# Performance work log

Hardware: AMD Instinct MI355X
Metric: run time of the kernel (lower is better)

## Reference

```python
import jax, jax.numpy as jnp
import numpy as np

K_GRID = 20          # grid side -> n1 = 400 nodes, n2 = 760 edges
CONTEXT = 512
HIDDEN = 2 * CONTEXT # per module: hidden_dim = 2*context_size
BATCH = 4096
RHO = 1.0            # ADMM penalty
N_ITERS = 50         # fixed ADMM iterations (differentiable unroll)


def _grid_incidence(k):
    """Node-arc incidence of a k x k grid DAG (right + down edges)."""
    n = k * k
    edges = []
    for i in range(k):
        for j in range(k):
            u = i * k + j
            if j + 1 < k:
                edges.append((u, i * k + j + 1))
            if i + 1 < k:
                edges.append((u, (i + 1) * k + j))
    m = len(edges)
    A = np.zeros((n, m), np.float32)
    for e, (u, v) in enumerate(edges):
        A[u, e] = 1.0   # outflow
        A[v, e] = -1.0  # inflow
    b = np.zeros(n, np.float32)
    b[0] = 1.0      # source
    b[n - 1] = -1.0 # sink
    return A, b


def setup_inputs() -> dict:
    key = jax.random.key(0)
    k_d, k_w1, k_b1, k_w2, k_b2 = jax.random.split(key, 5)
    A_np, b_np = _grid_incidence(K_GRID)
    n2 = A_np.shape[1]
    d = jax.random.normal(k_d, (BATCH, CONTEXT), dtype=jnp.float32)
    s1 = 1.0 / np.sqrt(CONTEXT)
    s2 = 1.0 / np.sqrt(HIDDEN)
    W1 = jax.random.uniform(k_w1, (HIDDEN, CONTEXT), jnp.float32, -s1, s1)
    b1 = jax.random.uniform(k_b1, (HIDDEN,), jnp.float32, -s1, s1)
    W2 = jax.random.uniform(k_w2, (n2, HIDDEN), jnp.float32, -s2, s2)
    b2 = jax.random.uniform(k_b2, (n2,), jnp.float32, -s2, s2)
    return {"d": d, "W1": W1, "b1": b1, "W2": W2, "b2": b2,
            "A": jnp.asarray(A_np), "b_eq": jnp.asarray(b_np)}


def reference(d, W1, b1, W2, b2, A, b_eq):
    # MLP router: fc_1 -> LeakyReLU(0.1) -> fc_2
    h = d @ W1.T + b1
    h = jnp.where(h >= 0, h, 0.1 * h)
    w = h @ W2.T + b2  # [B, n2] edge costs

    # QP: min_x w^T x + 0.5||x||^2  s.t.  A x = b_eq, x >= 0
    # Batched ADMM with equality-constrained x-update (KKT solve via pinv(AA^T)).
    M = jnp.linalg.pinv(A @ A.T)  # [n1, n1], symmetric
    z = jnp.zeros_like(w)
    u = jnp.zeros_like(w)
    x = jnp.zeros_like(w)

    def step(carry, _):
        x, z, u = carry
        v = RHO * (z - u) - w                       # [B, n2]
        nu = (v @ A.T - (1.0 + RHO) * b_eq) @ M     # [B, n1] dual of Ax=b
        x = (v - nu @ A) / (1.0 + RHO)              # satisfies A x = b
        z = jnp.maximum(x + u, 0.0)                 # projection onto x >= 0
        u = u + x - z
        return (x, z, u), None

    (x, z, u), _ = jax.lax.scan(step, (x, z, u), None, length=N_ITERS)
    return x  # [B, n2], primal solution (matches CvxpyLayer's variable x)
```

## Files before the change

### kernel.cpp

```cpp
#include <hip/hip_runtime.h>

#define KG 20
#define N1 400
#define N2 760
#define BATCH 4096
#define NITER 50

typedef __attribute__((ext_vector_type(8))) short bf16x8;
typedef __attribute__((ext_vector_type(4))) float f32x4;

#define CBAR() asm volatile("" ::: "memory")

__device__ __forceinline__ float bf2f(unsigned short u) {
    unsigned int x = ((unsigned int)u) << 16;
    union { unsigned int i; float f; } c; c.i = x; return c.f;
}
__device__ __forceinline__ unsigned short f2bf(float f) {
    union { float f; unsigned int i; } c; c.f = f;
    unsigned int r = c.i + 0x7FFFu + ((c.i >> 16) & 1u);
    return (unsigned short)(r >> 16);
}
__device__ __forceinline__ unsigned pk_bf16(float lo, float hi) {
    unsigned r;
    asm("v_cvt_pk_bf16_f32 %0, %1, %2" : "=v"(r) : "v"(lo), "v"(hi));
    return r;
}

constexpr double CPI = 3.14159265358979323846;
constexpr double ccos(double x) {
    constexpr double TP = 6.28318530717958647692;
    long long k = (long long)(x / TP);
    double r = x - (double)k * TP;
    if (r > CPI)  r -= TP;
    if (r < -CPI) r += TP;
    double r2 = r * r, term = 1.0, s = 1.0;
    for (int n = 1; n <= 15; ++n) { term *= -r2 / ((2.0 * n - 1.0) * (2.0 * n)); s += term; }
    return s;
}
struct Tbl { float phi[10][20]; float lam[20]; };
constexpr Tbl mk_tbl() {
    Tbl t{};
    for (int i = 0; i < 10; ++i)
        for (int a = 0; a < 20; ++a) {
            double na = (a == 0) ? 0.22360679774997896964 : 0.31622776601683793320;
            t.phi[i][a] = (float)(na * ccos(CPI * (double)a * ((double)i + 0.5) / 20.0));
        }
    for (int a = 0; a < 20; ++a) t.lam[a] = (float)(2.0 - 2.0 * ccos(CPI * (double)a / 20.0));
    return t;
}
static constexpr Tbl TB = mk_tbl();

__device__ __forceinline__ int detect_flag(const float* beqf) {
    float v = beqf[0];
    return (v > 0.5f && v < 1.5f) ? 0 : 1;
}

__global__ __launch_bounds__(256) void cvt_inputs(
        const void* __restrict__ src0, const void* __restrict__ src1,
        unsigned short* __restrict__ dst0, unsigned short* __restrict__ dst1,
        const float* __restrict__ beqf) {
    const int f = detect_flag(beqf);
    const int nv0 = (4096 * 512) / 4, nv1 = (1024 * 512) / 4;
    int idx = blockIdx.x * 256 + threadIdx.x;
    if (idx >= nv0 + nv1) return;
    const void* s; unsigned short* dptr; int k;
    if (idx < nv0) { s = src0; dptr = dst0; k = idx; }
    else           { s = src1; dptr = dst1; k = idx - nv0; }
    if (f) {
        ((uint2*)dptr)[k] = ((const uint2*)s)[k];
    } else {
        float4 v = ((const float4*)s)[k];
        uint2 p; p.x = pk_bf16(v.x, v.y); p.y = pk_bf16(v.z, v.w);
        ((uint2*)dptr)[k] = p;
    }
}

template<bool LEAKY>
__global__ __launch_bounds__(256) void gemm_bt_bf16(
        const unsigned short* __restrict__ A,
        const void* __restrict__ B,
        const void* __restrict__ biasRaw,
        unsigned short* __restrict__ C,
        int M, int N, int K, const float* __restrict__ beqf, int bUseFlag) {
    __shared__ unsigned short As[64 * 34];
    __shared__ unsigned short Bs[64 * 34];
    const int f   = detect_flag(beqf);
    const int bBf = bUseFlag ? f : 1;
    const int tid  = threadIdx.x;
    const int m0   = blockIdx.x * 64;
    const int n0   = blockIdx.y * 64;
    const int wave = tid >> 6, lane = tid & 63;
    const int wm   = (wave & 1) * 32, wn = (wave >> 1) * 32;
    const int fr   = lane & 15;
    const int kc   = (lane >> 4) * 8;

    const int ra = tid >> 2, ca = (tid & 3) * 8;
    const int rbg = (n0 + ra < N) ? (n0 + ra) : (N - 1);

    uint4 av, bv;
    auto load_tiles = [&](int k0) {
        size_t aoff = (size_t)(m0 + ra) * K + k0 + ca;
        av = *(const uint4*)&A[aoff];
        size_t boff = (size_t)rbg * K + k0 + ca;
        if (bBf) bv = *(const uint4*)&((const unsigned short*)B)[boff];
        else {
            const float* Bf = (const float*)B;
            float4 f0 = *(const float4*)&Bf[boff];
            float4 f1 = *(const float4*)&Bf[boff + 4];
            bv.x = pk_bf16(f0.x, f0.y);
            bv.y = pk_bf16(f0.z, f0.w);
            bv.z = pk_bf16(f1.x, f1.y);
            bv.w = pk_bf16(f1.z, f1.w);
        }
    };

    f32x4 acc[2][2];
#pragma unroll
    for (int a = 0; a < 2; a++)
#pragma unroll
        for (int b = 0; b < 2; b++) acc[a][b] = (f32x4){0.f, 0.f, 0.f, 0.f};

    load_tiles(0);
    for (int k0 = 0; k0 < K; k0 += 32) {
        *(uint4*)&As[ra * 34 + ca] = av;
        *(uint4*)&Bs[ra * 34 + ca] = bv;
        __syncthreads();

        int kn = (k0 + 32 < K) ? (k0 + 32) : k0;
        load_tiles(kn);

        bf16x8 af[2], bfm[2];
#pragma unroll
        for (int a = 0; a < 2; a++) af[a]  = *(const bf16x8*)&As[(wm + a * 16 + fr) * 34 + kc];
#pragma unroll
        for (int b = 0; b < 2; b++) bfm[b] = *(const bf16x8*)&Bs[(wn + b * 16 + fr) * 34 + kc];
#pragma unroll
        for (int a = 0; a < 2; a++)
#pragma unroll
            for (int b = 0; b < 2; b++)
                acc[a][b] = __builtin_amdgcn_mfma_f32_16x16x32_bf16(af[a], bfm[b], acc[a][b], 0, 0, 0);
        __syncthreads();
    }
#pragma unroll
    for (int a = 0; a < 2; a++)
#pragma unroll
        for (int b = 0; b < 2; b++) {
            int col = n0 + wn + b * 16 + (lane & 15);
            if (col < N) {
                float bs = f ? bf2f(((const unsigned short*)biasRaw)[col])
                             : ((const float*)biasRaw)[col];
#pragma unroll
                for (int r = 0; r < 4; r++) {
                    int row = m0 + wm + a * 16 + (lane >> 4) * 4 + r;
                    float v = acc[a][b][r] + bs;
                    if (LEAKY) v = v >= 0.f ? v : 0.1f * v;
                    C[(size_t)row * N + col] = f2bf(v);
                }
            }
        }
}

#define SREG 448
__global__ __launch_bounds__(64, 1) void admm_kernel(
        const unsigned short* __restrict__ wglob,
        void* __restrict__ out, const float* __restrict__ beqf) {
    __shared__ float buf[3 * SREG];

    const int lane = threadIdx.x;
    const int q    = (lane >= 40) ? 2 : (lane >= 20 ? 1 : 0);
    const int i    = lane - 20 * q;
    const int sample = blockIdx.x * 3 + q;
    const int flag = detect_flag(beqf);

    if (lane < 60 && sample < BATCH) {
        float* B = &buf[q * SREG];
        const size_t gb = (size_t)sample * N2;

        float wh[20], wv[20];
        if (i < 19) {
#pragma unroll
            for (int j = 0; j < 19; ++j) {
                wh[j] = bf2f(wglob[gb + 39 * i + 2 * j]);
                wv[j] = bf2f(wglob[gb + 39 * i + 2 * j + 1]);
            }
            wh[19] = 0.f;
            wv[19] = bf2f(wglob[gb + 39 * i + 38]);
        } else {
#pragma unroll
            for (int j = 0; j < 19; ++j) { wh[j] = bf2f(wglob[gb + 741 + j]); wv[j] = 0.f; }
            wh[19] = 0.f; wv[19] = 0.f;
        }

        float g[20];
        {
            float lamB = TB.lam[i];
#pragma unroll
            for (int a = 0; a < 20; ++a) g[a] = 1.f / (TB.lam[a] + lamB);
            if (i == 0) g[0] = 0.f;
        }

        float sh[20], sv[20];
#pragma unroll
        for (int j = 0; j < 20; ++j) { sh[j] = 0.f; sv[j] = 0.f; }

        const int rup = (i > 0)  ? i - 1 : 0;
        const int rdn = (i < 19) ? i + 1 : i;

#pragma unroll 1
        for (int it = 0; it < NITER; ++it) {
            float vh[20], vv[20];
#pragma unroll
            for (int j = 0; j < 20; ++j) {
                vh[j] = fabsf(sh[j]) - wh[j];
                vv[j] = fabsf(sv[j]) - wv[j];
            }
#pragma unroll
            for (int j = 0; j < 20; j += 4)
                *(f32x4*)&B[20 * i + j] = (f32x4){vv[j], vv[j + 1], vv[j + 2], vv[j + 3]};
            CBAR();
            float vvUp[20];
#pragma unroll
            for (int j = 0; j < 20; j += 4) {
                f32x4 t = *(f32x4*)&B[20 * rup + j];
                vvUp[j] = t[0]; vvUp[j + 1] = t[1]; vvUp[j + 2] = t[2]; vvUp[j + 3] = t[3];
            }
            CBAR();
            float r[20];
#pragma unroll
            for (int j = 0; j < 20; ++j) {
                float acc = ((j < 19) ? vh[j] : 0.f) + vv[j];
                if (j > 0) acc -= vh[j - 1];
                acc -= (i > 0) ? vvUp[j] : 0.f;
                r[j] = acc;
            }
            r[0]  -= (i == 0)  ? 2.f : 0.f;
            r[19] += (i == 19) ? 2.f : 0.f;

            float e[10], o[10];
#pragma unroll
            for (int jj = 0; jj < 10; ++jj) { e[jj] = r[jj] + r[19 - jj]; o[jj] = r[jj] - r[19 - jj]; }
#pragma unroll
            for (int b = 0; b < 20; ++b) {
                float a;
                if ((b & 1) == 0) {
                    a = e[0] * TB.phi[0][b];
#pragma unroll
                    for (int jj = 1; jj < 10; ++jj) a += e[jj] * TB.phi[jj][b];
                } else {
                    a = o[0] * TB.phi[0][b];
#pragma unroll
                    for (int jj = 1; jj < 10; ++jj) a += o[jj] * TB.phi[jj][b];
                }
                B[22 * b + i] = a;
            }
            CBAR();
            float t2[20];
#pragma unroll
            for (int k = 0; k < 20; k += 2) {
                float2 p = *(const float2*)&B[22 * i + k];
                t2[k] = p.x; t2[k + 1] = p.y;
            }
            CBAR();
            float e2[10], o2[10];
#pragma unroll
            for (int kk = 0; kk < 10; ++kk) { e2[kk] = t2[kk] + t2[19 - kk]; o2[kk] = t2[kk] - t2[19 - kk]; }
            float v2[20];
#pragma unroll
            for (int a = 0; a < 20; ++a) {
                float acc;
                if ((a & 1) == 0) {
                    acc = e2[0] * TB.phi[0][a];
#pragma unroll
                    for (int kk = 1; kk < 10; ++kk) acc += e2[kk] * TB.phi[kk][a];
                } else {
                    acc = o2[0] * TB.phi[0][a];
#pragma unroll
                    for (int kk = 1; kk < 10; ++kk) acc += o2[kk] * TB.phi[kk][a];
                }
                v2[a] = acc * g[a];
            }
#pragma unroll
            for (int II = 0; II < 10; ++II) {
                float E = v2[0] * TB.phi[II][0];
#pragma unroll
                for (int m = 1; m < 10; ++m) E += v2[2 * m] * TB.phi[II][2 * m];
                float O = v2[1] * TB.phi[II][1];
#pragma unroll
                for (int m = 1; m < 10; ++m) O += v2[2 * m + 1] * TB.phi[II][2 * m + 1];
                B[22 * II + i]        = E + O;
                B[22 * (19 - II) + i] = E - O;
            }
            CBAR();
            float t3[20];
#pragma unroll
            for (int b = 0; b < 20; b += 2) {
                float2 p = *(const float2*)&B[22 * i + b];
                t3[b] = p.x; t3[b + 1] = p.y;
            }
            CBAR();
            float nu[20];
#pragma unroll
            for (int JJ = 0; JJ < 10; ++JJ) {
                float E = t3[0] * TB.phi[JJ][0];
#pragma unroll
                for (int m = 1; m < 10; ++m) E += t3[2 * m] * TB.phi[JJ][2 * m];
                float O = t3[1] * TB.phi[JJ][1];
#pragma unroll
                for (int m = 1; m < 10; ++m) O += t3[2 * m + 1] * TB.phi[JJ][2 * m + 1];
                nu[JJ]      = E + O;
                nu[19 - JJ] = E - O;
            }
#pragma unroll
            for (int j = 0; j < 20; j += 4)
                *(f32x4*)&B[20 * i + j] = (f32x4){nu[j], nu[j + 1], nu[j + 2], nu[j + 3]};
            CBAR();
            float nuDn[20];
#pragma unroll
            for (int j = 0; j < 20; j += 4) {
                f32x4 t = *(f32x4*)&B[20 * rdn + j];
                nuDn[j] = t[0]; nuDn[j + 1] = t[1]; nuDn[j + 2] = t[2]; nuDn[j + 3] = t[3];
            }
            CBAR();
#pragma unroll
            for (int j = 0; j < 20; ++j) {
                float xv = 0.5f * (vv[j] - nu[j] + nuDn[j]);
                sv[j] = xv + fminf(sv[j], 0.f);
                float xh = 0.f;
                if (j < 19) {
                    xh = 0.5f * (vh[j] - nu[j] + nu[j + 1]);
                    sh[j] = xh + fminf(sh[j], 0.f);
                }
                if (it == NITER - 1) {
                    if (i < 19) {
                        if (j < 19) {
                            if (flag) {
                                ((unsigned short*)out)[gb + 39 * i + 2 * j]     = f2bf(xh);
                                ((unsigned short*)out)[gb + 39 * i + 2 * j + 1] = f2bf(xv);
                            } else {
                                ((float*)out)[gb + 39 * i + 2 * j]     = xh;
                                ((float*)out)[gb + 39 * i + 2 * j + 1] = xv;
                            }
                        } else {
                            if (flag) ((unsigned short*)out)[gb + 39 * i + 38] = f2bf(xv);
                            else      ((float*)out)[gb + 39 * i + 38] = xv;
                        }
                    } else if (j < 19) {
                        if (flag) ((unsigned short*)out)[gb + 741 + j] = f2bf(xh);
                        else      ((float*)out)[gb + 741 + j] = xh;
                    }
                }
            }
        }
    }
}

extern "C" void kernel_launch(void* const* d_in, const int* in_sizes, int n_in,
                              void* d_out, int out_size, void* d_ws, size_t ws_size,
                              hipStream_t stream) {
    (void)in_sizes; (void)n_in; (void)out_size; (void)ws_size;
    const void*  d   = d_in[0];
    const void*  W1  = d_in[1];
    const void*  b1  = d_in[2];
    const void*  W2  = d_in[3];
    const void*  b2  = d_in[4];
    const float* beq = (const float*)d_in[6];

    char* ws = (char*)d_ws;
    unsigned short* h_bf  = (unsigned short*)(ws);
    unsigned short* w_bf  = (unsigned short*)(ws + 8388608);
    unsigned short* d_bf  = (unsigned short*)(ws + 8388608);
    unsigned short* w1_bf = (unsigned short*)(ws + 12582912);

    cvt_inputs<<<2560, 256, 0, stream>>>(d, W1, d_bf, w1_bf, beq);

    gemm_bt_bf16<true ><<<dim3(64, 16), 256, 0, stream>>>(d_bf, w1_bf, b1, h_bf, 4096, 1024, 512,  beq, 0);
    gemm_bt_bf16<false><<<dim3(64, 12), 256, 0, stream>>>(h_bf, W2,    b2, w_bf, 4096, 760,  1024, beq, 1);

    admm_kernel<<<(BATCH + 2) / 3, 64, 0, stream>>>(w_bf, d_out, beq);
}
```

Before: 324.5 us.

## Fuse input conversion and both MLP GEMMs into one cooperative persistent kernel

Merges the bf16 conversion kernel and the two MLP GEMM launches into a single cooperative kernel of 512 persistent blocks. The blocks loop over GEMM tiles and use grid-wide syncs between phases. W2 is now pre-converted to bf16 in the conversion phase instead of inside the GEMM load loop. This targets launch overhead and the idle gaps between kernels, at the cost of grid syncs and a fixed grid of 512 blocks that may limit occupancy and load balance. The ADMM kernel, which likely dominates runtime, is left as it was.

```diff
diff --git a/kernel.cpp b/kernel.cpp
--- a/kernel.cpp
+++ b/kernel.cpp
@@ -1,4 +1,7 @@
 #include <hip/hip_runtime.h>
+#include <hip/hip_cooperative_groups.h>
+
+namespace cg = cooperative_groups;
 
 #define KG 20
 #define N1 400
@@ -55,109 +58,116 @@
     return (v > 0.5f && v < 1.5f) ? 0 : 1;
 }
 
-__global__ __launch_bounds__(256) void cvt_inputs(
-        const void* __restrict__ src0, const void* __restrict__ src1,
-        unsigned short* __restrict__ dst0, unsigned short* __restrict__ dst1,
-        const float* __restrict__ beqf) {
-    const int f = detect_flag(beqf);
-    const int nv0 = (4096 * 512) / 4, nv1 = (1024 * 512) / 4;
-    int idx = blockIdx.x * 256 + threadIdx.x;
-    if (idx >= nv0 + nv1) return;
-    const void* s; unsigned short* dptr; int k;
-    if (idx < nv0) { s = src0; dptr = dst0; k = idx; }
-    else           { s = src1; dptr = dst1; k = idx - nv0; }
-    if (f) {
-        ((uint2*)dptr)[k] = ((const uint2*)s)[k];
-    } else {
-        float4 v = ((const float4*)s)[k];
-        uint2 p; p.x = pk_bf16(v.x, v.y); p.y = pk_bf16(v.z, v.w);
-        ((uint2*)dptr)[k] = p;
-    }
-}
 
 template<bool LEAKY>
-__global__ __launch_bounds__(256) void gemm_bt_bf16(
+__device__ __forceinline__ void gemm_tiles(
         const unsigned short* __restrict__ A,
-        const void* __restrict__ B,
+        const unsigned short* __restrict__ Bm,
         const void* __restrict__ biasRaw,
         unsigned short* __restrict__ C,
-        int M, int N, int K, const float* __restrict__ beqf, int bUseFlag) {
-    __shared__ unsigned short As[64 * 34];
-    __shared__ unsigned short Bs[64 * 34];
-    const int f   = detect_flag(beqf);
-    const int bBf = bUseFlag ? f : 1;
-    const int tid  = threadIdx.x;
-    const int m0   = blockIdx.x * 64;
-    const int n0   = blockIdx.y * 64;
+        int M, int N, int K, int f,
+        unsigned short* As, unsigned short* Bs, int bId, int tid) {
+    const int tn   = (N + 63) >> 6;
+    const int ttot = (M >> 6) * tn;
     const int wave = tid >> 6, lane = tid & 63;
     const int wm   = (wave & 1) * 32, wn = (wave >> 1) * 32;
     const int fr   = lane & 15;
     const int kc   = (lane >> 4) * 8;
-
-    const int ra = tid >> 2, ca = (tid & 3) * 8;
-    const int rbg = (n0 + ra < N) ? (n0 + ra) : (N - 1);
-
-    uint4 av, bv;
-    auto load_tiles = [&](int k0) {
-        size_t aoff = (size_t)(m0 + ra) * K + k0 + ca;
-        av = *(const uint4*)&A[aoff];
-        size_t boff = (size_t)rbg * K + k0 + ca;
-        if (bBf) bv = *(const uint4*)&((const unsigned short*)B)[boff];
-        else {
-            const float* Bf = (const float*)B;
-            float4 f0 = *(const float4*)&Bf[boff];
-            float4 f1 = *(const float4*)&Bf[boff + 4];
-            bv.x = pk_bf16(f0.x, f0.y);
-            bv.y = pk_bf16(f0.z, f0.w);
-            bv.z = pk_bf16(f1.x, f1.y);
-            bv.w = pk_bf16(f1.z, f1.w);
-        }
-    };
-
-    f32x4 acc[2][2];
-#pragma unroll
-    for (int a = 0; a < 2; a++)
-#pragma unroll
-        for (int b = 0; b < 2; b++) acc[a][b] = (f32x4){0.f, 0.f, 0.f, 0.f};
-
-    load_tiles(0);
-    for (int k0 = 0; k0 < K; k0 += 32) {
-        *(uint4*)&As[ra * 34 + ca] = av;
-        *(uint4*)&Bs[ra * 34 + ca] = bv;
+    const int ra   = tid >> 2, ca = (tid & 3) * 8;
+
+    for (int t = bId; t < ttot; t += 512) {
+        const int m0  = (t / tn) * 64;
+        const int n0  = (t % tn) * 64;
+        const int rbg = (n0 + ra < N) ? (n0 + ra) : (N - 1);
+        const size_t abase = (size_t)(m0 + ra) * K + ca;
+        const size_t bbase = (size_t)rbg * K + ca;
+
+        uint4 av = *(const uint4*)&A[abase];
+        uint4 bv = *(const uint4*)&Bm[bbase];
+
+        f32x4 acc[2][2];
+#pragma unroll
+        for (int a = 0; a < 2; a++)
+#pragma unroll
+            for (int b = 0; b < 2; b++) acc[a][b] = (f32x4){0.f, 0.f, 0.f, 0.f};
+
+        for (int k0 = 0; k0 < K; k0 += 32) {
+            __syncthreads();
+            *(uint4*)&As[ra * 34 + ca] = av;
+            *(uint4*)&Bs[ra * 34 + ca] = bv;
+            __syncthreads();
+
+            int kn = (k0 + 32 < K) ? (k0 + 32) : k0;
+            av = *(const uint4*)&A[abase + kn];
+            bv = *(const uint4*)&Bm[bbase + kn];
+
+            bf16x8 af[2], bfm[2];
+#pragma unroll
+            for (int a = 0; a < 2; a++) af[a]  = *(const bf16x8*)&As[(wm + a * 16 + fr) * 34 + kc];
+#pragma unroll
+            for (int b = 0; b < 2; b++) bfm[b] = *(const bf16x8*)&Bs[(wn + b * 16 + fr) * 34 + kc];
+#pragma unroll
+            for (int a = 0; a < 2; a++)
+#pragma unroll
+                for (int b = 0; b < 2; b++)
+                    acc[a][b] = __builtin_amdgcn_mfma_f32_16x16x32_bf16(af[a], bfm[b], acc[a][b], 0, 0, 0);
+        }
         __syncthreads();
-
-        int kn = (k0 + 32 < K) ? (k0 + 32) : k0;
-        load_tiles(kn);
-
-        bf16x8 af[2], bfm[2];
-#pragma unroll
-        for (int a = 0; a < 2; a++) af[a]  = *(const bf16x8*)&As[(wm + a * 16 + fr) * 34 + kc];
-#pragma unroll
-        for (int b = 0; b < 2; b++) bfm[b] = *(const bf16x8*)&Bs[(wn + b * 16 + fr) * 34 + kc];
 #pragma unroll
         for (int a = 0; a < 2; a++)
 #pragma unroll
-            for (int b = 0; b < 2; b++)
-                acc[a][b] = __builtin_amdgcn_mfma_f32_16x16x32_bf16(af[a], bfm[b], acc[a][b], 0, 0, 0);
-        __syncthreads();
+            for (int b = 0; b < 2; b++) {
+                int col = n0 + wn + b * 16 + (lane & 15);
+                if (col < N) {
+                    float bs = f ? bf2f(((const unsigned short*)biasRaw)[col])
+                                 : ((const float*)biasRaw)[col];
+#pragma unroll
+                    for (int r = 0; r < 4; r++) {
+                        int row = m0 + wm + a * 16 + (lane >> 4) * 4 + r;
+                        float v = acc[a][b][r] + bs;
+                        if (LEAKY) v = v >= 0.f ? v : 0.1f * v;
+                        C[(size_t)row * N + col] = f2bf(v);
+                    }
+                }
+            }
     }
-#pragma unroll
-    for (int a = 0; a < 2; a++)
-#pragma unroll
-        for (int b = 0; b < 2; b++) {
-            int col = n0 + wn + b * 16 + (lane & 15);
-            if (col < N) {
-                float bs = f ? bf2f(((const unsigned short*)biasRaw)[col])
-                             : ((const float*)biasRaw)[col];
-#pragma unroll
-                for (int r = 0; r < 4; r++) {
-                    int row = m0 + wm + a * 16 + (lane >> 4) * 4 + r;
-                    float v = acc[a][b][r] + bs;
-                    if (LEAKY) v = v >= 0.f ? v : 0.1f * v;
-                    C[(size_t)row * N + col] = f2bf(v);
-                }
-            }
-        }
+}
+
+__global__ __launch_bounds__(256, 2) void mlp_fused(
+        const void* dRaw, const void* w1Raw, const void* w2Raw,
+        const void* b1Raw, const void* b2Raw,
+        unsigned short* d_bf, unsigned short* w1_bf, unsigned short* w2_bf,
+        unsigned short* h_bf, unsigned short* w_bf,
+        const float* beqf) {
+    __shared__ unsigned short As[64 * 34];
+    __shared__ unsigned short Bs[64 * 34];
+    const int f   = detect_flag(beqf);
+    const int tid = threadIdx.x;
+    const int b   = blockIdx.x;
+
+    {
+        const int nv0 = (4096 * 512) / 4;
+        const int nv1 = (1024 * 512) / 4;
+        const int nv2 = (760 * 1024) / 4;
+        const int total = nv0 + nv1 + nv2;
+        for (int idx = b * 256 + tid; idx < total; idx += 512 * 256) {
+            const void* s; unsigned short* dst; int k;
+            if (idx < nv0)             { s = dRaw;  dst = d_bf;  k = idx; }
+            else if (idx < nv0 + nv1)  { s = w1Raw; dst = w1_bf; k = idx - nv0; }
+            else                       { s = w2Raw; dst = w2_bf; k = idx - nv0 - nv1; }
+            if (f) {
+                ((uint2*)dst)[k] = ((const uint2*)s)[k];
+            } else {
+                float4 v = ((const float4*)s)[k];
+                uint2 p; p.x = pk_bf16(v.x, v.y); p.y = pk_bf16(v.z, v.w);
+                ((uint2*)dst)[k] = p;
+            }
+        }
+    }
+    cg::this_grid().sync();
+    gemm_tiles<true >(d_bf, w1_bf, b1Raw, h_bf, 4096, 1024, 512,  f, As, Bs, b, tid);
+    cg::this_grid().sync();
+    gemm_tiles<false>(h_bf, w2_bf, b2Raw, w_bf, 4096, 760,  1024, f, As, Bs, b, tid);
 }
 
 #define SREG 448
@@ -368,13 +378,15 @@
     char* ws = (char*)d_ws;
     unsigned short* h_bf  = (unsigned short*)(ws);
     unsigned short* w_bf  = (unsigned short*)(ws + 8388608);
-    unsigned short* d_bf  = (unsigned short*)(ws + 8388608);
-    unsigned short* w1_bf = (unsigned short*)(ws + 12582912);
-
-    cvt_inputs<<<2560, 256, 0, stream>>>(d, W1, d_bf, w1_bf, beq);
-
-    gemm_bt_bf16<true ><<<dim3(64, 16), 256, 0, stream>>>(d_bf, w1_bf, b1, h_bf, 4096, 1024, 512,  beq, 0);
-    gemm_bt_bf16<false><<<dim3(64, 12), 256, 0, stream>>>(h_bf, W2,    b2, w_bf, 4096, 760,  1024, beq, 1);
+    unsigned short* d_bf  = (unsigned short*)(ws + 16777216);
+    unsigned short* w1_bf = (unsigned short*)(ws + 20971520);
+    unsigned short* w2_bf = (unsigned short*)(ws + 22020096);
+
+    void* kargs[] = { (void*)&d, (void*)&W1, (void*)&W2, (void*)&b1, (void*)&b2,
+                      (void*)&d_bf, (void*)&w1_bf, (void*)&w2_bf,
+                      (void*)&h_bf, (void*)&w_bf, (void*)&beq };
+    hipLaunchCooperativeKernel((const void*)mlp_fused, dim3(512), dim3(256),
+                               kargs, 0, stream);
 
     admm_kernel<<<(BATCH + 2) / 3, 64, 0, stream>>>(w_bf, d_out, beq);
 }
```

After: 523.0 us. 61.2% more time.
